# Kernel tuning notes

Measured on AMD Instinct MI355X. Metric: run time of the kernel, lower is better.

The kernel has to match this reference:

```python
import jax, jax.numpy as jnp
import numpy as np

STATE_DIM = 1024
ACTION_DIM = 512
TASK_DIM = 64
EMBED = 64
HID = 128
B = 256


def setup_inputs() -> dict:
    key = jax.random.key(0)
    ks = jax.random.split(key, 24)
    s = 0.02
    inp = {
        "obs": jax.random.normal(ks[0], (B, STATE_DIM), dtype=jnp.float32),
        "task_label": jax.random.normal(ks[1], (B, TASK_DIM), dtype=jnp.float32),
        "action": jax.random.randint(ks[2], (B,), 0, ACTION_DIM, dtype=jnp.int64 if jax.config.jax_enable_x64 else jnp.int32),
        # task encoder: Linear(64,64) ReLU Linear(64,64) ReLU
        "we1": jax.random.normal(ks[3], (TASK_DIM, EMBED)) * s,
        "be1": jnp.zeros((EMBED,), jnp.float32),
        "we2": jax.random.normal(ks[4], (EMBED, EMBED)) * s,
        "be2": jnp.zeros((EMBED,), jnp.float32),
        # h_action net_W: Linear(64,128) ReLU Linear(128, 512*1024)
        "aw1": jax.random.normal(ks[5], (EMBED, HID)) * s,
        "aw1b": jnp.zeros((HID,), jnp.float32),
        "aw2": jax.random.normal(ks[6], (HID, ACTION_DIM * STATE_DIM)) * s,
        "aw2b": jnp.zeros((ACTION_DIM * STATE_DIM,), jnp.float32),
        # h_action net_b: Linear(64,128) ReLU Linear(128, 512)
        "ab1": jax.random.normal(ks[7], (EMBED, HID)) * s,
        "ab1b": jnp.zeros((HID,), jnp.float32),
        "ab2": jax.random.normal(ks[8], (HID, ACTION_DIM)) * s,
        "ab2b": jnp.zeros((ACTION_DIM,), jnp.float32),
        # h_critic net_W: Linear(64,128) ReLU Linear(128, 1*1024)
        "cw1": jax.random.normal(ks[9], (EMBED, HID)) * s,
        "cw1b": jnp.zeros((HID,), jnp.float32),
        "cw2": jax.random.normal(ks[10], (HID, 1 * STATE_DIM)) * s,
        "cw2b": jnp.zeros((STATE_DIM,), jnp.float32),
        # h_critic net_b: Linear(64,128) ReLU Linear(128, 1)
        "cb1": jax.random.normal(ks[11], (EMBED, HID)) * s,
        "cb1b": jnp.zeros((HID,), jnp.float32),
        "cb2": jax.random.normal(ks[12], (HID, 1)) * s,
        "cb2b": jnp.zeros((1,), jnp.float32),
    }
    return inp


def reference(obs, task_label, action, we1, be1, we2, be2,
              aw1, aw1b, aw2, aw2b, ab1, ab1b, ab2, ab2b,
              cw1, cw1b, cw2, cw2b, cb1, cb1b, cb2, cb2b):
    relu = jax.nn.relu
    b = obs.shape[0]
    # DummyBody: phi = phi_a = phi_v = obs
    # task encoder -> z [B, EMBED]
    z = relu(relu(task_label @ we1 + be1) @ we2 + be2)
    # hypernet-generated actor head: W [B, A, S], b [B, A]
    Wa = (relu(z @ aw1 + aw1b) @ aw2 + aw2b).reshape(b, ACTION_DIM, STATE_DIM)
    ba = relu(z @ ab1 + ab1b) @ ab2 + ab2b
    # hypernet-generated critic head: W [B, 1, S], b [B, 1]
    Wv = (relu(z @ cw1 + cw1b) @ cw2 + cw2b).reshape(b, 1, STATE_DIM)
    bv = relu(z @ cb1 + cb1b) @ cb2 + cb2b
    # bmm apply (torch.bmm(W, phi.unsqueeze(-1)).squeeze(-1) + b)
    logits = jnp.einsum('boi,bi->bo', Wa, obs) + ba
    v = jnp.einsum('boi,bi->bo', Wv, obs) + bv
    logp = jax.nn.log_softmax(logits, axis=-1)
    log_prob = jnp.take_along_axis(logp, action[:, None].astype(jnp.int32), axis=-1)  # [B,1]
    entropy = -jnp.sum(jnp.exp(logp) * logp, axis=-1, keepdims=True)  # [B,1]
    return logits, action, log_prob, entropy, v
```

## Files before the change

kernel.cpp:

```cpp
#include <hip/hip_runtime.h>
#include <hip/hip_bf16.h>

#define B_SZ 256
#define SDIM 1024
#define ADIM 512

#define NCHUNK 16
#define RING 5

typedef __attribute__((ext_vector_type(8))) short bf16x8;
typedef __attribute__((ext_vector_type(4))) float f32x4;

__device__ __forceinline__ unsigned short f2bf(float x) {
  union { float f; unsigned u; } v; v.f = x;
  unsigned r = v.u + 0x7FFFu + ((v.u >> 16) & 1u);
  return (unsigned short)(r >> 16);
}

__device__ __forceinline__ void gll16(const void* g, void* l) {
  __builtin_amdgcn_global_load_lds(
      (const __attribute__((address_space(1))) unsigned int*)g,
      (__attribute__((address_space(3))) unsigned int*)l, 16, 0, 0);
}

__device__ __forceinline__ unsigned cvtpk(float lo, float hi) {
  unsigned r;
  asm("v_cvt_pk_bf16_f32 %0, %1, %2" : "=v"(r) : "v"(lo), "v"(hi));
  return r;
}

__global__ __launch_bounds__(128) void kprep(
    const float* __restrict__ obs,
    const float* __restrict__ task, const int* __restrict__ action,
    const float* __restrict__ we1, const float* __restrict__ be1,
    const float* __restrict__ we2, const float* __restrict__ be2,
    const float* __restrict__ aw1, const float* __restrict__ aw1b,
    const float* __restrict__ ab1, const float* __restrict__ ab1b,
    const float* __restrict__ ab2, const float* __restrict__ ab2b,
    const float* __restrict__ cw1, const float* __restrict__ cw1b,
    const float* __restrict__ cb1, const float* __restrict__ cb1b,
    const float* __restrict__ cb2, const float* __restrict__ cb2b,
    const float* __restrict__ cw2b,
    float* __restrict__ ws_ha, float* __restrict__ ws_hc,
    unsigned short* __restrict__ obsT,
    float* __restrict__ out)
{
  const int b = blockIdx.x, t = threadIdx.x;
  __shared__ float s_task[64], s_t1[64], s_z[64], s_hb[128], s_red[128];

  float dotc = 0.0f;
  {
    const int kc = t >> 2, g = t & 3;
    const float4* src = (const float4*)(obs + (size_t)b * SDIM + kc * 32 + g * 8);
    const float4* cbp = (const float4*)(cw2b + kc * 32 + g * 8);
    float4 x = src[0], y = src[1];
    float4 c0 = cbp[0], c1 = cbp[1];
    dotc = x.x * c0.x + x.y * c0.y + x.z * c0.z + x.w * c0.w
         + y.x * c1.x + y.y * c1.y + y.z * c1.z + y.w * c1.w;
    ushort4 u0, u1;
    u0.x = f2bf(x.x); u0.y = f2bf(x.y); u0.z = f2bf(x.z); u0.w = f2bf(x.w);
    u1.x = f2bf(y.x); u1.y = f2bf(y.y); u1.z = f2bf(y.z); u1.w = f2bf(y.w);
    ushort4* d = (ushort4*)(obsT + ((size_t)(kc * 4 + g) * 256 + b) * 8);
    d[0] = u0; d[1] = u1;
  }

  if (t < 64) s_task[t] = task[b * 64 + t];
  __syncthreads();
  if (t < 64) {
    float a = be1[t];
    for (int e = 0; e < 64; ++e) a += s_task[e] * we1[e * 64 + t];
    s_t1[t] = fmaxf(a, 0.0f);
  }
  __syncthreads();
  if (t < 64) {
    float a = be2[t];
    for (int e = 0; e < 64; ++e) a += s_t1[e] * we2[e * 64 + t];
    s_z[t] = fmaxf(a, 0.0f);
  }
  __syncthreads();
  {
    float a1 = aw1b[t], a2 = ab1b[t], a3 = cw1b[t], a4 = cb1b[t];
    for (int e = 0; e < 64; ++e) {
      const float zv = s_z[e];
      a1 += zv * aw1[e * 128 + t];
      a2 += zv * ab1[e * 128 + t];
      a3 += zv * cw1[e * 128 + t];
      a4 += zv * cb1[e * 128 + t];
    }
    ws_ha[b * 128 + t] = fmaxf(a1, 0.0f);
    s_hb[t] = fmaxf(a2, 0.0f);
    ws_hc[b * 128 + t] = fmaxf(a3, 0.0f);
    s_red[t] = fmaxf(a4, 0.0f) * cb2[t] + dotc;
  }
  __syncthreads();
  for (int o = t; o < ADIM; o += 128) {
    float a = ab2b[o];
    for (int h = 0; h < 128; ++h) a += s_hb[h] * ab2[h * ADIM + o];
    out[b * ADIM + o] = a;
  }
  for (int s = 64; s > 0; s >>= 1) {
    __syncthreads();
    if (t < s) s_red[t] += s_red[t + s];
  }
  if (t == 0) {
    out[131840 + b] = s_red[0] + cb2b[0];
    out[131072 + b] = (float)action[b];
  }
}

__global__ __launch_bounds__(512, 1) void khyper(
    const unsigned short* __restrict__ obsT,
    const float* __restrict__ aw2, const float* __restrict__ aw2b,
    const float* __restrict__ cw2,
    const float* __restrict__ ws_ha, const float* __restrict__ ws_hc,
    float* __restrict__ d_out)
{
  __shared__ __align__(16) char ring[RING * 16384];
  __shared__ unsigned sync[80];

  const int tid = threadIdx.x, blk = blockIdx.x;
  const int wv = tid >> 6, lane = tid & 63;
  const int lrow = lane & 15, grp = lane >> 4;

  int wtype, o0 = 0, kq;
  const char* rowbase;
  size_t rowstride;
  if (blk < 1024) {
    wtype = 0; o0 = blk >> 1; kq = blk & 1;
    rowbase = (const char*)(aw2 + (size_t)o0 * SDIM);
    rowstride = (size_t)ADIM * SDIM * 4;
  } else if (blk < 1032) {
    const int idx = blk - 1024;
    wtype = 1; o0 = (idx >> 1) * 128; kq = idx & 1;
    rowbase = (const char*)(aw2b + (size_t)o0 * SDIM);
    rowstride = SDIM * 4;
  } else {
    wtype = 2; kq = blk - 1032;
    rowbase = (const char*)cw2;
    rowstride = SDIM * 4;
  }

  if (tid < 80) sync[tid] = 0;
  __syncthreads();

  if (wv >= 4) {
    const int w = wv - 4;
    const char* src[4];
#pragma unroll
    for (int j = 0; j < 4; ++j) {
      const int row = 32 * w + 8 * j + (lane >> 3);
      const int slot = lane & 7;
      src[j] = rowbase + (size_t)row * rowstride + kq * 2048
             + ((slot ^ (row & 7)) << 4);
    }
#pragma unroll 1
    for (int c = 0; c < NCHUNK; ++c) {
      if (c >= RING) {
        while (*(volatile unsigned*)&sync[64 + c - RING] < 4u)
          __builtin_amdgcn_s_sleep(2);
      }
      char* dst = ring + (c % RING) * 16384 + w * 4096;
#pragma unroll
      for (int j = 0; j < 4; ++j)
        gll16(src[j] + (size_t)c * 128, dst + j * 1024);
      if (c >= 4) {
        asm volatile("s_waitcnt vmcnt(16)" ::: "memory");
        *(volatile unsigned*)&sync[(c - 4) * 4 + w] = 1;
      }
    }
    asm volatile("s_waitcnt vmcnt(12)" ::: "memory");
    *(volatile unsigned*)&sync[12 * 4 + w] = 1;
    asm volatile("s_waitcnt vmcnt(8)" ::: "memory");
    *(volatile unsigned*)&sync[13 * 4 + w] = 1;
    asm volatile("s_waitcnt vmcnt(4)" ::: "memory");
    *(volatile unsigned*)&sync[14 * 4 + w] = 1;
    asm volatile("s_waitcnt vmcnt(0)" ::: "memory");
    *(volatile unsigned*)&sync[15 * 4 + w] = 1;
    return;
  }

  const int m0 = wv * 64;
  const unsigned short* pA[4];
#pragma unroll
  for (int mf = 0; mf < 4; ++mf)
    pA[mf] = obsT + (((size_t)(kq * 16) * 4 + grp) * 256 + (m0 + mf * 16 + lrow)) * 8;

  int boff[8][2];
#pragma unroll
  for (int nf = 0; nf < 8; ++nf) {
    const int row = nf * 16 + lrow;
#pragma unroll
    for (int q = 0; q < 2; ++q)
      boff[nf][q] = row * 128 + (((2 * grp + q) ^ (row & 7)) << 4);
  }

  f32x4 acc[4][8];
#pragma unroll
  for (int mf = 0; mf < 4; ++mf)
#pragma unroll
    for (int nf = 0; nf < 8; ++nf) acc[mf][nf] = (f32x4)(0.0f);

#pragma unroll 1
  for (int c = 0; c < NCHUNK; ++c) {
    {
      const volatile unsigned* fl = &sync[c * 4];
      while (fl[0] == 0u || fl[1] == 0u || fl[2] == 0u || fl[3] == 0u)
        __builtin_amdgcn_s_sleep(2);
    }
    const char* wb = ring + (c % RING) * 16384;
    bf16x8 af[4];
#pragma unroll
    for (int mf = 0; mf < 4; ++mf)
      af[mf] = *(const bf16x8*)(pA[mf] + (size_t)c * 8192);
#pragma unroll
    for (int nf = 0; nf < 8; ++nf) {
      f32x4 x = *(const f32x4*)(wb + boff[nf][0]);
      f32x4 y = *(const f32x4*)(wb + boff[nf][1]);
      union { bf16x8 v; unsigned u[4]; } p;
      p.u[0] = cvtpk(x[0], x[1]); p.u[1] = cvtpk(x[2], x[3]);
      p.u[2] = cvtpk(y[0], y[1]); p.u[3] = cvtpk(y[2], y[3]);
#pragma unroll
      for (int mf = 0; mf < 4; ++mf)
        acc[mf][nf] = __builtin_amdgcn_mfma_f32_16x16x32_bf16(af[mf], p.v, acc[mf][nf], 0, 0, 0);
    }
    asm volatile("s_waitcnt lgkmcnt(0)" ::: "memory");
    if (lane == 0) atomicAdd(&sync[64 + c], 1u);
  }

  if (wtype == 1) {
#pragma unroll
    for (int mf = 0; mf < 4; ++mf) {
      const int b = m0 + mf * 16 + grp * 4;
#pragma unroll
      for (int nf = 0; nf < 8; ++nf) {
        const int col = o0 + nf * 16 + lrow;
#pragma unroll
        for (int r = 0; r < 4; ++r)
          atomicAdd(&d_out[(size_t)(b + r) * ADIM + col], acc[mf][nf][r]);
      }
    }
  } else {
    const float* hw = (wtype == 0) ? ws_ha : ws_hc;
#pragma unroll
    for (int mf = 0; mf < 4; ++mf) {
      const int b = m0 + mf * 16 + grp * 4;
      float val[4] = {0.f, 0.f, 0.f, 0.f};
#pragma unroll
      for (int nf = 0; nf < 8; ++nf) {
        const int h = nf * 16 + lrow;
#pragma unroll
        for (int r = 0; r < 4; ++r)
          val[r] += hw[(size_t)(b + r) * 128 + h] * acc[mf][nf][r];
      }
#pragma unroll
      for (int r = 0; r < 4; ++r) {
        float v = val[r];
        v += __shfl_xor(v, 1, 64);
        v += __shfl_xor(v, 2, 64);
        v += __shfl_xor(v, 4, 64);
        v += __shfl_xor(v, 8, 64);
        val[r] = v;
      }
      if (lrow == 0) {
#pragma unroll
        for (int r = 0; r < 4; ++r) {
          if (wtype == 0) atomicAdd(&d_out[(size_t)(b + r) * ADIM + o0], val[r]);
          else            atomicAdd(&d_out[131840 + b + r], val[r]);
        }
      }
    }
  }
}

__global__ __launch_bounds__(256) void kfinal(const int* __restrict__ action,
                                              float* __restrict__ d_out)
{
  const int b = blockIdx.x, t = threadIdx.x;
  const float* lrow = d_out + (size_t)b * ADIM;
  __shared__ float sM[4], sS[4], sT[4];

  const float x0 = lrow[t], x1 = lrow[t + 256];
  float m = fmaxf(x0, x1);
#pragma unroll
  for (int s = 1; s < 64; s <<= 1) m = fmaxf(m, __shfl_xor(m, s, 64));
  const int wv = t >> 6, ln = t & 63;
  if (ln == 0) sM[wv] = m;
  __syncthreads();
  m = fmaxf(fmaxf(sM[0], sM[1]), fmaxf(sM[2], sM[3]));

  const float d0 = x0 - m, d1 = x1 - m;
  const float e0 = expf(d0), e1 = expf(d1);
  float s1 = e0 + e1;
  float s2 = e0 * d0 + e1 * d1;
#pragma unroll
  for (int s = 1; s < 64; s <<= 1) {
    s1 += __shfl_xor(s1, s, 64);
    s2 += __shfl_xor(s2, s, 64);
  }
  if (ln == 0) { sS[wv] = s1; sT[wv] = s2; }
  __syncthreads();
  if (t == 0) {
    const float S = sS[0] + sS[1] + sS[2] + sS[3];
    const float T = sT[0] + sT[1] + sT[2] + sT[3];
    const float lnS = logf(S);
    const int a = action[b];
    d_out[131328 + b] = (lrow[a] - m) - lnS;
    d_out[131584 + b] = lnS - T / S;
  }
}

extern "C" void kernel_launch(void* const* d_in, const int* in_sizes, int n_in,
                              void* d_out_v, int out_size, void* d_ws, size_t ws_size,
                              hipStream_t stream) {
  const float* obs   = (const float*)d_in[0];
  const float* task  = (const float*)d_in[1];
  const int*   action= (const int*)  d_in[2];
  const float* we1   = (const float*)d_in[3];
  const float* be1   = (const float*)d_in[4];
  const float* we2   = (const float*)d_in[5];
  const float* be2   = (const float*)d_in[6];
  const float* aw1   = (const float*)d_in[7];
  const float* aw1b  = (const float*)d_in[8];
  const float* aw2   = (const float*)d_in[9];
  const float* aw2b  = (const float*)d_in[10];
  const float* ab1   = (const float*)d_in[11];
  const float* ab1b  = (const float*)d_in[12];
  const float* ab2   = (const float*)d_in[13];
  const float* ab2b  = (const float*)d_in[14];
  const float* cw1   = (const float*)d_in[15];
  const float* cw1b  = (const float*)d_in[16];
  const float* cw2   = (const float*)d_in[17];
  const float* cw2b  = (const float*)d_in[18];
  const float* cb1   = (const float*)d_in[19];
  const float* cb1b  = (const float*)d_in[20];
  const float* cb2   = (const float*)d_in[21];
  const float* cb2b  = (const float*)d_in[22];
  float* out = (float*)d_out_v;
  float* ws_ha = (float*)d_ws;
  float* ws_hc = ws_ha + 256 * 128;
  unsigned short* obsT = (unsigned short*)(ws_hc + 256 * 128);

  kprep<<<256, 128, 0, stream>>>(obs, task, action, we1, be1, we2, be2, aw1, aw1b,
                                 ab1, ab1b, ab2, ab2b, cw1, cw1b, cb1, cb1b,
                                 cb2, cb2b, cw2b, ws_ha, ws_hc, obsT, out);
  khyper<<<1034, 512, 0, stream>>>(obsT, aw2, aw2b, cw2, ws_ha, ws_hc, out);
  kfinal<<<256, 256, 0, stream>>>(action, out);
}
```

Before: 168.5 us.

## Split K into four quarters and stream row-chunks instead of K-chunks

Each block now handles a quarter of the K dimension (256 elements) instead of half, doubling the grid to 2068 blocks. The producer waves stream 32-row chunks that each span the full 1KB K-slice, where before they streamed narrow K-slices across all 128 rows. The consumer loop is fully unrolled, uses the chunk index to pick the accumulator column, and places a sched_barrier after each wait. Small aw2b/cw2 blocks are moved to the front of the grid. This trades more partial-sum reduction work and more LDS per block (96KB ring) for more parallelism and longer contiguous row reads.

```diff
diff --git a/kernel.cpp b/kernel.cpp
--- a/kernel.cpp
+++ b/kernel.cpp
@@ -5,8 +5,8 @@
 #define SDIM 1024
 #define ADIM 512
 
-#define NCHUNK 16
-#define RING 5
+#define NCHUNK 4
+#define RING 3
 
 typedef __attribute__((ext_vector_type(8))) short bf16x8;
 typedef __attribute__((ext_vector_type(4))) float f32x4;
@@ -115,8 +115,8 @@
     const float* __restrict__ ws_ha, const float* __restrict__ ws_hc,
     float* __restrict__ d_out)
 {
-  __shared__ __align__(16) char ring[RING * 16384];
-  __shared__ unsigned sync[80];
+  __shared__ __align__(16) char ring[RING * 32768];
+  __shared__ unsigned sync[20];
 
   const int tid = threadIdx.x, blk = blockIdx.x;
   const int wv = tid >> 6, lane = tid & 63;
@@ -125,74 +125,56 @@
   int wtype, o0 = 0, kq;
   const char* rowbase;
   size_t rowstride;
-  if (blk < 1024) {
-    wtype = 0; o0 = blk >> 1; kq = blk & 1;
+  if (blk < 16) {
+    wtype = 1; o0 = (blk >> 2) * 128; kq = blk & 3;
+    rowbase = (const char*)(aw2b + (size_t)o0 * SDIM);
+    rowstride = SDIM * 4;
+  } else if (blk < 20) {
+    wtype = 2; kq = blk - 16;
+    rowbase = (const char*)cw2;
+    rowstride = SDIM * 4;
+  } else {
+    const int idx = blk - 20;
+    wtype = 0; o0 = idx >> 2; kq = idx & 3;
     rowbase = (const char*)(aw2 + (size_t)o0 * SDIM);
     rowstride = (size_t)ADIM * SDIM * 4;
-  } else if (blk < 1032) {
-    const int idx = blk - 1024;
-    wtype = 1; o0 = (idx >> 1) * 128; kq = idx & 1;
-    rowbase = (const char*)(aw2b + (size_t)o0 * SDIM);
-    rowstride = SDIM * 4;
-  } else {
-    wtype = 2; kq = blk - 1032;
-    rowbase = (const char*)cw2;
-    rowstride = SDIM * 4;
-  }
-
-  if (tid < 80) sync[tid] = 0;
+  }
+  const size_t kbyte = (size_t)kq * 1024;
+
+  if (tid < 20) sync[tid] = 0;
   __syncthreads();
 
   if (wv >= 4) {
     const int w = wv - 4;
-    const char* src[4];
-#pragma unroll
-    for (int j = 0; j < 4; ++j) {
-      const int row = 32 * w + 8 * j + (lane >> 3);
-      const int slot = lane & 7;
-      src[j] = rowbase + (size_t)row * rowstride + kq * 2048
-             + ((slot ^ (row & 7)) << 4);
-    }
-#pragma unroll 1
+#pragma unroll
     for (int c = 0; c < NCHUNK; ++c) {
       if (c >= RING) {
-        while (*(volatile unsigned*)&sync[64 + c - RING] < 4u)
+        while (*(volatile unsigned*)&sync[16 + c - RING] < 4u)
           __builtin_amdgcn_s_sleep(2);
       }
-      char* dst = ring + (c % RING) * 16384 + w * 4096;
-#pragma unroll
-      for (int j = 0; j < 4; ++j)
-        gll16(src[j] + (size_t)c * 128, dst + j * 1024);
-      if (c >= 4) {
-        asm volatile("s_waitcnt vmcnt(16)" ::: "memory");
-        *(volatile unsigned*)&sync[(c - 4) * 4 + w] = 1;
-      }
-    }
-    asm volatile("s_waitcnt vmcnt(12)" ::: "memory");
-    *(volatile unsigned*)&sync[12 * 4 + w] = 1;
-    asm volatile("s_waitcnt vmcnt(8)" ::: "memory");
-    *(volatile unsigned*)&sync[13 * 4 + w] = 1;
-    asm volatile("s_waitcnt vmcnt(4)" ::: "memory");
-    *(volatile unsigned*)&sync[14 * 4 + w] = 1;
+      char* dst = ring + (c % RING) * 32768 + w * 8192;
+#pragma unroll
+      for (int j = 0; j < 8; ++j) {
+        const int row = c * 32 + w * 8 + j;
+        const char* s = rowbase + (size_t)row * rowstride + kbyte
+                      + (size_t)((lane ^ (row & 7)) << 4);
+        gll16(s, dst + j * 1024);
+      }
+      if (c >= 1) {
+        asm volatile("s_waitcnt vmcnt(8)" ::: "memory");
+        *(volatile unsigned*)&sync[(c - 1) * 4 + w] = 1;
+      }
+    }
     asm volatile("s_waitcnt vmcnt(0)" ::: "memory");
-    *(volatile unsigned*)&sync[15 * 4 + w] = 1;
+    *(volatile unsigned*)&sync[(NCHUNK - 1) * 4 + w] = 1;
     return;
   }
 
   const int m0 = wv * 64;
-  const unsigned short* pA[4];
+  const unsigned short* pA0[4];
 #pragma unroll
   for (int mf = 0; mf < 4; ++mf)
-    pA[mf] = obsT + (((size_t)(kq * 16) * 4 + grp) * 256 + (m0 + mf * 16 + lrow)) * 8;
-
-  int boff[8][2];
-#pragma unroll
-  for (int nf = 0; nf < 8; ++nf) {
-    const int row = nf * 16 + lrow;
-#pragma unroll
-    for (int q = 0; q < 2; ++q)
-      boff[nf][q] = row * 128 + (((2 * grp + q) ^ (row & 7)) << 4);
-  }
+    pA0[mf] = obsT + (((size_t)(kq * 8) * 4 + grp) * 256 + (m0 + mf * 16 + lrow)) * 8;
 
   f32x4 acc[4][8];
 #pragma unroll
@@ -200,31 +182,39 @@
 #pragma unroll
     for (int nf = 0; nf < 8; ++nf) acc[mf][nf] = (f32x4)(0.0f);
 
-#pragma unroll 1
+#pragma unroll
   for (int c = 0; c < NCHUNK; ++c) {
     {
       const volatile unsigned* fl = &sync[c * 4];
       while (fl[0] == 0u || fl[1] == 0u || fl[2] == 0u || fl[3] == 0u)
         __builtin_amdgcn_s_sleep(2);
     }
-    const char* wb = ring + (c % RING) * 16384;
-    bf16x8 af[4];
-#pragma unroll
-    for (int mf = 0; mf < 4; ++mf)
-      af[mf] = *(const bf16x8*)(pA[mf] + (size_t)c * 8192);
-#pragma unroll
-    for (int nf = 0; nf < 8; ++nf) {
-      f32x4 x = *(const f32x4*)(wb + boff[nf][0]);
-      f32x4 y = *(const f32x4*)(wb + boff[nf][1]);
-      union { bf16x8 v; unsigned u[4]; } p;
-      p.u[0] = cvtpk(x[0], x[1]); p.u[1] = cvtpk(x[2], x[3]);
-      p.u[2] = cvtpk(y[0], y[1]); p.u[3] = cvtpk(y[2], y[3]);
+    __builtin_amdgcn_sched_barrier(0);
+    const char* wb = ring + (c % RING) * 32768;
+#pragma unroll
+    for (int ks = 0; ks < 8; ++ks) {
+      bf16x8 af[4];
 #pragma unroll
       for (int mf = 0; mf < 4; ++mf)
-        acc[mf][nf] = __builtin_amdgcn_mfma_f32_16x16x32_bf16(af[mf], p.v, acc[mf][nf], 0, 0, 0);
+        af[mf] = *(const bf16x8*)(pA0[mf] + (size_t)ks * 8192);
+#pragma unroll
+      for (int nfl = 0; nfl < 2; ++nfl) {
+        const int row_local = nfl * 16 + lrow;
+        const int s0 = (ks * 8 + grp * 2 + 0) ^ (row_local & 7);
+        const int s1 = (ks * 8 + grp * 2 + 1) ^ (row_local & 7);
+        f32x4 x = *(const f32x4*)(wb + row_local * 1024 + (s0 << 4));
+        f32x4 y = *(const f32x4*)(wb + row_local * 1024 + (s1 << 4));
+        union { bf16x8 v; unsigned u[4]; } p;
+        p.u[0] = cvtpk(x[0], x[1]); p.u[1] = cvtpk(x[2], x[3]);
+        p.u[2] = cvtpk(y[0], y[1]); p.u[3] = cvtpk(y[2], y[3]);
+#pragma unroll
+        for (int mf = 0; mf < 4; ++mf)
+          acc[mf][c * 2 + nfl] =
+              __builtin_amdgcn_mfma_f32_16x16x32_bf16(af[mf], p.v, acc[mf][c * 2 + nfl], 0, 0, 0);
+      }
     }
     asm volatile("s_waitcnt lgkmcnt(0)" ::: "memory");
-    if (lane == 0) atomicAdd(&sync[64 + c], 1u);
+    if (lane == 0) atomicAdd(&sync[16 + c], 1u);
   }
 
   if (wtype == 1) {
@@ -343,6 +333,6 @@
   kprep<<<256, 128, 0, stream>>>(obs, task, action, we1, be1, we2, be2, aw1, aw1b,
                                  ab1, ab1b, ab2, ab2b, cw1, cw1b, cb1, cb1b,
                                  cb2, cb2b, cw2b, ws_ha, ws_hc, obsT, out);
-  khyper<<<1034, 512, 0, stream>>>(obsT, aw2, aw2b, cw2, ws_ha, ws_hc, out);
+  khyper<<<2068, 512, 0, stream>>>(obsT, aw2, aw2b, cw2, ws_ha, ws_hc, out);
   kfinal<<<256, 256, 0, stream>>>(action, out);
 }
```

Result: slower. 179.3 us (+6.4%).
